# Kernel tuning notes

Hardware: AMD Instinct MI355X
Metric: run time of the kernel (lower is better)

The kernel has to match this reference:

```python
import jax, jax.numpy as jnp
import numpy as np

NEG_INF = -9e15
ALPHA = 0.2  # LeakyReLU negative slope

N = 8192
D_IN = 512
D_OUT = 256


def setup_inputs() -> dict:
    key = jax.random.key(0)
    k1, k2, k3, k4, k5 = jax.random.split(key, 5)
    features = jax.random.normal(k1, (N, D_IN), dtype=jnp.float32)
    adjacency_matrix = jax.random.randint(k2, (N, N), 0, 2, dtype=jnp.int32)
    # learned params (torch Linear stores [out, in]; we use [in, out] layout)
    s_phi = 1.0 / np.sqrt(D_IN)
    W_phi = jax.random.uniform(k3, (D_IN, D_OUT), jnp.float32, -s_phi, s_phi)
    s_v = 1.0 / np.sqrt(D_OUT)
    w_mu = jax.random.uniform(k4, (D_OUT,), jnp.float32, -s_v, s_v)
    w_xi = jax.random.uniform(k5, (D_OUT,), jnp.float32, -s_v, s_v)
    return {"features": features, "adjacency_matrix": adjacency_matrix,
            "W_phi": W_phi, "w_mu": w_mu, "w_xi": w_xi}


def reference(features, adjacency_matrix, W_phi, w_mu, w_xi):
    h = features @ W_phi                                   # [N, d_out]
    mu = h @ w_mu                                          # [N]
    xi = h @ w_xi                                          # [N]
    e = mu[:, None] + xi[None, :]                          # [N, N] additive scores
    e = jnp.where(e >= 0, e, ALPHA * e)                    # LeakyReLU
    e = jnp.where(adjacency_matrix > 0, e, NEG_INF)        # mask non-edges
    a = jax.nn.softmax(e, axis=1)                          # row softmax (dropout p=0)
    out = a @ h                                            # weighted aggregation
    return jax.nn.elu(out)
```

## Files before the change

### kernel.cpp

```cpp
#include <hip/hip_runtime.h>
#include <cstdint>
#include <cstddef>


#define LOG2E 1.44269504f

typedef __attribute__((ext_vector_type(8))) short short8;
typedef __attribute__((ext_vector_type(4))) float floatx4;

using uint_as1 = __attribute__((address_space(1))) unsigned int;
using uint_as3 = __attribute__((address_space(3))) unsigned int;

__device__ __forceinline__ void gld_lds16(const void* g, void* l) {
  __builtin_amdgcn_global_load_lds((const uint_as1*)g, (uint_as3*)l, 16, 0, 0);
}

__device__ __forceinline__ unsigned short f2b(float f) {
  unsigned u = __float_as_uint(f);
  u += 0x7fffu + ((u >> 16) & 1u);
  return (unsigned short)(u >> 16);
}

__device__ __forceinline__ unsigned cvtpk_bf16(float a, float b) {
  unsigned r;
  asm("v_cvt_pk_bf16_f32 %0, %1, %2" : "=v"(r) : "v"(a), "v"(b));
  return r;
}

__global__ void k_prep_wt(const float* __restrict__ w, unsigned short* __restrict__ wt) {
  int tid = blockIdx.x * 256 + threadIdx.x;
  int n = tid >> 9, k = tid & 511;
  wt[n * 512 + k] = f2b(w[k * 256 + n]);
}

__global__ __launch_bounds__(256, 2) void k_gemm1m(const float* __restrict__ f,
                                                   const unsigned short* __restrict__ wt,
                                                   const float* __restrict__ wmu,
                                                   const float* __restrict__ wxi,
                                                   unsigned short* __restrict__ ht,
                                                   float* __restrict__ mupart,
                                                   float* __restrict__ xipart) {
  __shared__ __align__(16) unsigned short As[64 * 64];
  __shared__ __align__(16) unsigned short Bs[128 * 64];
  __shared__ float musum[4][64];
  __shared__ float xisum[4][64];
  int t = threadIdx.x, w = t >> 6, l = t & 63;
  int bm_ = blockIdx.x >> 1, bn = blockIdx.x & 1;
  int m0 = bm_ * 64, n0 = bn * 128;
  int lr = l >> 3, lg = l & 7, g = lg ^ lr;
  int kg = l >> 4, ln = l & 15;
  floatx4 zero = {0.f, 0.f, 0.f, 0.f};
  floatx4 acc[4][2];
#pragma unroll
  for (int mf = 0; mf < 4; ++mf)
#pragma unroll
    for (int nf = 0; nf < 2; ++nf) acc[mf][nf] = zero;

  for (int it = 0; it < 8; ++it) {
    int k0 = it * 64;
#pragma unroll
    for (int q = 0; q < 2; ++q) {
      int row = w * 16 + q * 8 + lr;
      const float* fp = f + (size_t)(m0 + row) * 512 + k0 + g * 8;
      float4 v0 = *(const float4*)fp;
      float4 v1 = *(const float4*)(fp + 4);
      uint4 d = {cvtpk_bf16(v0.x, v0.y), cvtpk_bf16(v0.z, v0.w),
                 cvtpk_bf16(v1.x, v1.y), cvtpk_bf16(v1.z, v1.w)};
      *(uint4*)&As[row * 64 + lg * 8] = d;
    }
#pragma unroll
    for (int q = 0; q < 4; ++q) {
      int row = w * 32 + q * 8 + lr;
      const void* gp = wt + (size_t)(n0 + row) * 512 + k0 + g * 8;
      int lb = __builtin_amdgcn_readfirstlane((w * 32 + q * 8) * 64);
      gld_lds16(gp, &Bs[lb]);
    }
    __syncthreads();
#pragma unroll
    for (int ks = 0; ks < 2; ++ks) {
      int gg = ks * 4 + kg;
      int swz = (gg ^ (ln & 7)) * 8;
      short8 bfr[2];
#pragma unroll
      for (int nf = 0; nf < 2; ++nf)
        bfr[nf] = *(const short8*)&Bs[(w * 32 + nf * 16 + ln) * 64 + swz];
#pragma unroll
      for (int mf = 0; mf < 4; ++mf) {
        short8 afr = *(const short8*)&As[(mf * 16 + ln) * 64 + swz];
#pragma unroll
        for (int nf = 0; nf < 2; ++nf)
          acc[mf][nf] = __builtin_amdgcn_mfma_f32_16x16x32_bf16(afr, bfr[nf], acc[mf][nf], 0, 0, 0);
      }
    }
    __syncthreads();
  }
#pragma unroll
  for (int mf = 0; mf < 4; ++mf)
#pragma unroll
    for (int nf = 0; nf < 2; ++nf) {
      int ng = n0 + w * 32 + nf * 16 + ln;
      int mg = m0 + mf * 16 + kg * 4;
      ushort4 o = {f2b(acc[mf][nf][0]), f2b(acc[mf][nf][1]),
                   f2b(acc[mf][nf][2]), f2b(acc[mf][nf][3])};
      *(ushort4*)&ht[(size_t)ng * 8192 + mg] = o;
    }
  float wma = wmu[n0 + w * 32 + ln], wmb = wmu[n0 + w * 32 + 16 + ln];
  float wxa = wxi[n0 + w * 32 + ln], wxb = wxi[n0 + w * 32 + 16 + ln];
#pragma unroll
  for (int mf = 0; mf < 4; ++mf)
#pragma unroll
    for (int r = 0; r < 4; ++r) {
      float ms = acc[mf][0][r] * wma + acc[mf][1][r] * wmb;
      float xs = acc[mf][0][r] * wxa + acc[mf][1][r] * wxb;
      ms += __shfl_xor(ms, 1); ms += __shfl_xor(ms, 2);
      ms += __shfl_xor(ms, 4); ms += __shfl_xor(ms, 8);
      xs += __shfl_xor(xs, 1); xs += __shfl_xor(xs, 2);
      xs += __shfl_xor(xs, 4); xs += __shfl_xor(xs, 8);
      if (ln == 0) {
        musum[w][mf * 16 + kg * 4 + r] = ms;
        xisum[w][mf * 16 + kg * 4 + r] = xs;
      }
    }
  __syncthreads();
  if (t < 64) {
    float m_ = musum[0][t] + musum[1][t] + musum[2][t] + musum[3][t];
    mupart[(size_t)bn * 8192 + m0 + t] = m_;
  } else if (t < 128) {
    int r = t - 64;
    float x_ = xisum[0][r] + xisum[1][r] + xisum[2][r] + xisum[3][r];
    xipart[(size_t)bn * 8192 + m0 + r] = x_;
  }
}

__global__ __launch_bounds__(512, 1) void k_gatt16(const int* __restrict__ adjm,
                                                   const unsigned short* __restrict__ ht,
                                                   const float* __restrict__ mupart,
                                                   const float* __restrict__ xipart,
                                                   float* __restrict__ nump,
                                                   float* __restrict__ zpart) {
  __shared__ __align__(16) unsigned short Bs[4][256 * 32];
  __shared__ __align__(16) float EfE[1024];
  __shared__ __align__(16) float EfF[1024];

  int t = threadIdx.x, w = t >> 6, l = t & 63;
  int ln = l & 15, kg = l >> 4;
  int jb = blockIdx.x & 7, ig = blockIdx.x >> 3;
  int i0 = ig * 256;
  int jc0 = jb * 1024;

  {
    int t2 = t & 255;
    float4 xa = *(const float4*)&xipart[jc0 + t2 * 4];
    float4 xb = *(const float4*)&xipart[8192 + jc0 + t2 * 4];
    float x0 = (xa.x + xb.x) * LOG2E, x1 = (xa.y + xb.y) * LOG2E;
    float x2 = (xa.z + xb.z) * LOG2E, x3 = (xa.w + xb.w) * LOG2E;
    if (t < 256) {
      EfE[t2 * 4 + 0] = __builtin_amdgcn_exp2f(x0);
      EfE[t2 * 4 + 1] = __builtin_amdgcn_exp2f(x1);
      EfE[t2 * 4 + 2] = __builtin_amdgcn_exp2f(x2);
      EfE[t2 * 4 + 3] = __builtin_amdgcn_exp2f(x3);
    } else {
      EfF[t2 * 4 + 0] = __builtin_amdgcn_exp2f(0.2f * x0);
      EfF[t2 * 4 + 1] = __builtin_amdgcn_exp2f(0.2f * x1);
      EfF[t2 * 4 + 2] = __builtin_amdgcn_exp2f(0.2f * x2);
      EfF[t2 * 4 + 3] = __builtin_amdgcn_exp2f(0.2f * x3);
    }
  }

  float EM[2], FM[2];
#pragma unroll
  for (int mf = 0; mf < 2; ++mf) {
    int i = i0 + w * 32 + mf * 16 + ln;
    float mu = (mupart[i] + mupart[8192 + i]) * LOG2E;
    EM[mf] = __builtin_amdgcn_exp2f(mu);
    FM[mf] = __builtin_amdgcn_exp2f(0.2f * mu);
  }

  const int* ar0 = adjm + (size_t)(i0 + w * 32 + ln) * 8192 + jc0 + kg * 8;
  const int* ar1 = ar0 + (size_t)16 * 8192;

  floatx4 zero = {0.f, 0.f, 0.f, 0.f};
  floatx4 acc[2][16];
#pragma unroll
  for (int mf = 0; mf < 2; ++mf)
#pragma unroll
    for (int nf = 0; nf < 16; ++nf) acc[mf][nf] = zero;
  float zacc[2] = {0.f, 0.f};

#define STAGE_B(win_, b_)                                                   \
  {                                                                         \
    int j0_ = jc0 + (win_) * 32;                                            \
    _Pragma("unroll")                                                       \
    for (int q = 0; q < 2; ++q) {                                           \
      int rowbase = w * 32 + q * 16;                                        \
      int row = rowbase + (l >> 2);                                         \
      int g = (l & 3) ^ ((row >> 1) & 3);                                   \
      const void* gp = ht + (size_t)row * 8192 + j0_ + g * 8;               \
      int lb = __builtin_amdgcn_readfirstlane((b_) * (256 * 32) + rowbase * 32); \
      gld_lds16(gp, &((unsigned short*)Bs)[lb]);                            \
    }                                                                       \
  }

  STAGE_B(0, 0);
  STAGE_B(1, 1);
  __syncthreads();

  for (int win = 0; win < 32; ++win) {
    int bR = win & 3;
    if (win < 31) {
      asm volatile("s_waitcnt vmcnt(2)" ::: "memory");
    } else {
      asm volatile("s_waitcnt vmcnt(0)" ::: "memory");
    }
    __builtin_amdgcn_s_barrier();
    asm volatile("" ::: "memory");

    int joff = win * 32;
    int4 a0 = *(const int4*)(ar0 + joff);
    int4 a1 = *(const int4*)(ar0 + joff + 4);
    int4 a2 = *(const int4*)(ar1 + joff);
    int4 a3 = *(const int4*)(ar1 + joff + 4);

    int jl = win * 32 + kg * 8;
    float4 e0 = *(const float4*)&EfE[jl];
    float4 e1 = *(const float4*)&EfE[jl + 4];
    float4 f0 = *(const float4*)&EfF[jl];
    float4 f1 = *(const float4*)&EfF[jl + 4];

    short8 af[2];
#pragma unroll
    for (int mf = 0; mf < 2; ++mf) {
      int av[8];
      if (mf == 0) {
        av[0] = a0.x; av[1] = a0.y; av[2] = a0.z; av[3] = a0.w;
        av[4] = a1.x; av[5] = a1.y; av[6] = a1.z; av[7] = a1.w;
      } else {
        av[0] = a2.x; av[1] = a2.y; av[2] = a2.z; av[3] = a2.w;
        av[4] = a3.x; av[5] = a3.y; av[6] = a3.z; av[7] = a3.w;
      }
      float ex[8] = {e0.x, e0.y, e0.z, e0.w, e1.x, e1.y, e1.z, e1.w};
      float fx[8] = {f0.x, f0.y, f0.z, f0.w, f1.x, f1.y, f1.z, f1.w};
      float A = EM[mf], F = FM[mf];
      union { unsigned u[4]; short8 s; } cv;
      float zs = 0.f;
#pragma unroll
      for (int p = 0; p < 4; ++p) {
        float m0 = fmaxf(A * ex[2 * p], F * fx[2 * p]);
        float m1 = fmaxf(A * ex[2 * p + 1], F * fx[2 * p + 1]);
        m0 = (av[2 * p] != 0) ? m0 : 0.f;
        m1 = (av[2 * p + 1] != 0) ? m1 : 0.f;
        zs += m0;
        zs += m1;
        cv.u[p] = cvtpk_bf16(m0, m1);
      }
      zacc[mf] += zs;
      af[mf] = cv.s;
    }
#pragma unroll
    for (int qtr = 0; qtr < 4; ++qtr) {
      short8 bfv[4];
#pragma unroll
      for (int nf = 0; nf < 4; ++nf) {
        int n = qtr * 64 + nf * 16 + ln;
        bfv[nf] = *(const short8*)&Bs[bR][n * 32 + ((kg ^ ((n >> 1) & 3)) * 8)];
      }
#pragma unroll
      for (int mf = 0; mf < 2; ++mf)
#pragma unroll
        for (int nf = 0; nf < 4; ++nf)
          acc[mf][qtr * 4 + nf] = __builtin_amdgcn_mfma_f32_16x16x32_bf16(
              af[mf], bfv[nf], acc[mf][qtr * 4 + nf], 0, 0, 0);
    }
    if (win < 30) {
      STAGE_B(win + 2, (win + 2) & 3);
    }
  }
#undef STAGE_B

#pragma unroll
  for (int mf = 0; mf < 2; ++mf) {
    float z = zacc[mf];
    z += __shfl_xor(z, 16);
    z += __shfl_xor(z, 32);
    if (l < 16) zpart[(size_t)jb * 8192 + i0 + w * 32 + mf * 16 + ln] = z;
  }

  float* np = nump + (size_t)jb * (8192 * 256);
#pragma unroll
  for (int mf = 0; mf < 2; ++mf) {
    int rowb = i0 + w * 32 + mf * 16 + kg * 4;
#pragma unroll
    for (int r = 0; r < 4; ++r) {
      float* rp = np + (size_t)(rowb + r) * 256;
#pragma unroll
      for (int nf = 0; nf < 16; ++nf)
        rp[nf * 16 + ln] = acc[mf][nf][r];
    }
  }
}

__global__ void k_final(const float* __restrict__ nump, const float* __restrict__ zpart,
                        float* __restrict__ out) {
  int tid = blockIdx.x * 256 + threadIdx.x;
  int i = tid >> 6;
  float z = 0.f;
#pragma unroll
  for (int p = 0; p < 8; ++p) z += zpart[(size_t)p * 8192 + i];
  float zi = 1.0f / z;
  float4 v = {0.f, 0.f, 0.f, 0.f};
#pragma unroll
  for (int p = 0; p < 8; ++p) {
    float4 s = *(const float4*)&nump[(size_t)p * (8192 * 256) + tid * 4];
    v.x += s.x; v.y += s.y; v.z += s.z; v.w += s.w;
  }
  v.x *= zi; v.y *= zi; v.z *= zi; v.w *= zi;
  v.x = (v.x > 0.f) ? v.x : (__builtin_amdgcn_exp2f(v.x * LOG2E) - 1.f);
  v.y = (v.y > 0.f) ? v.y : (__builtin_amdgcn_exp2f(v.y * LOG2E) - 1.f);
  v.z = (v.z > 0.f) ? v.z : (__builtin_amdgcn_exp2f(v.z * LOG2E) - 1.f);
  v.w = (v.w > 0.f) ? v.w : (__builtin_amdgcn_exp2f(v.w * LOG2E) - 1.f);
  *(float4*)&out[tid * 4] = v;
}

extern "C" void kernel_launch(void* const* d_in, const int* in_sizes, int n_in,
                              void* d_out, int out_size, void* d_ws, size_t ws_size,
                              hipStream_t stream) {
  const float* features = (const float*)d_in[0];
  const int* adjm = (const int*)d_in[1];
  const float* W_phi = (const float*)d_in[2];
  const float* w_mu = (const float*)d_in[3];
  const float* w_xi = (const float*)d_in[4];
  float* out = (float*)d_out;

  char* ws = (char*)d_ws;
  unsigned short* ht  = (unsigned short*)(ws + 0);
  unsigned short* wt  = (unsigned short*)(ws + 4194304);
  float* mupart = (float*)(ws + 4456448);
  float* xipart = (float*)(ws + 4521984);
  float* zpart  = (float*)(ws + 4587520);
  float* nump   = (float*)(ws + 8388608);

  k_prep_wt<<<512, 256, 0, stream>>>(W_phi, wt);
  k_gemm1m<<<256, 256, 0, stream>>>(features, wt, w_mu, w_xi, ht, mupart, xipart);
  k_gatt16<<<256, 512, 0, stream>>>(adjm, ht, mupart, xipart, nump, zpart);
  k_final<<<2048, 256, 0, stream>>>(nump, zpart, out);
}
```

Baseline: 447.7 us.

## Fuse split-K reduction and ELU into attention kernel with in-block wave split

Restructures the attention kernel so each block owns 32 rows and its 8 waves split the 8192-wide neighbour dimension, reducing partial accumulators through shared memory and applying normalization and ELU in-kernel. This removes the partial-numerator buffer writes (8×8192×256 floats), the global zpart round trip and the separate final kernel launch. B fragments are now read directly from global memory without LDS staging, adjacency loads are software-prefetched one step ahead, and the whole exp table is rebuilt per block. Risks: uncached global B loads per MFMA, a serialized multi-step LDS tree reduction, and a single wave doing the final output writes.

```diff
diff --git a/kernel.cpp b/kernel.cpp
--- a/kernel.cpp
+++ b/kernel.cpp
@@ -132,52 +132,48 @@
   }
 }
 
-__global__ __launch_bounds__(512, 1) void k_gatt16(const int* __restrict__ adjm,
+__global__ __launch_bounds__(512, 1) void k_gatt17(const int* __restrict__ adjm,
                                                    const unsigned short* __restrict__ ht,
                                                    const float* __restrict__ mupart,
                                                    const float* __restrict__ xipart,
-                                                   float* __restrict__ nump,
-                                                   float* __restrict__ zpart) {
-  __shared__ __align__(16) unsigned short Bs[4][256 * 32];
-  __shared__ __align__(16) float EfE[1024];
-  __shared__ __align__(16) float EfF[1024];
+                                                   float* __restrict__ out) {
+  __shared__ __align__(16) char smem[131072];
+  __shared__ __align__(16) float zb[8][32];
+  __shared__ float zinv_s[32];
+
+  float* EfE = (float*)smem;
+  float* EfF = (float*)(smem + 32768);
 
   int t = threadIdx.x, w = t >> 6, l = t & 63;
   int ln = l & 15, kg = l >> 4;
-  int jb = blockIdx.x & 7, ig = blockIdx.x >> 3;
-  int i0 = ig * 256;
-  int jc0 = jb * 1024;
-
-  {
-    int t2 = t & 255;
-    float4 xa = *(const float4*)&xipart[jc0 + t2 * 4];
-    float4 xb = *(const float4*)&xipart[8192 + jc0 + t2 * 4];
+  int i0 = blockIdx.x * 32;
+  int jw0 = w * 1024;
+
+#pragma unroll
+  for (int q = 0; q < 4; ++q) {
+    int idx = q * 2048 + t * 4;
+    float4 xa = *(const float4*)&xipart[idx];
+    float4 xb = *(const float4*)&xipart[8192 + idx];
     float x0 = (xa.x + xb.x) * LOG2E, x1 = (xa.y + xb.y) * LOG2E;
     float x2 = (xa.z + xb.z) * LOG2E, x3 = (xa.w + xb.w) * LOG2E;
-    if (t < 256) {
-      EfE[t2 * 4 + 0] = __builtin_amdgcn_exp2f(x0);
-      EfE[t2 * 4 + 1] = __builtin_amdgcn_exp2f(x1);
-      EfE[t2 * 4 + 2] = __builtin_amdgcn_exp2f(x2);
-      EfE[t2 * 4 + 3] = __builtin_amdgcn_exp2f(x3);
-    } else {
-      EfF[t2 * 4 + 0] = __builtin_amdgcn_exp2f(0.2f * x0);
-      EfF[t2 * 4 + 1] = __builtin_amdgcn_exp2f(0.2f * x1);
-      EfF[t2 * 4 + 2] = __builtin_amdgcn_exp2f(0.2f * x2);
-      EfF[t2 * 4 + 3] = __builtin_amdgcn_exp2f(0.2f * x3);
-    }
-  }
-
+    EfE[idx + 0] = __builtin_amdgcn_exp2f(x0);
+    EfE[idx + 1] = __builtin_amdgcn_exp2f(x1);
+    EfE[idx + 2] = __builtin_amdgcn_exp2f(x2);
+    EfE[idx + 3] = __builtin_amdgcn_exp2f(x3);
+    EfF[idx + 0] = __builtin_amdgcn_exp2f(0.2f * x0);
+    EfF[idx + 1] = __builtin_amdgcn_exp2f(0.2f * x1);
+    EfF[idx + 2] = __builtin_amdgcn_exp2f(0.2f * x2);
+    EfF[idx + 3] = __builtin_amdgcn_exp2f(0.2f * x3);
+  }
   float EM[2], FM[2];
 #pragma unroll
   for (int mf = 0; mf < 2; ++mf) {
-    int i = i0 + w * 32 + mf * 16 + ln;
+    int i = i0 + mf * 16 + ln;
     float mu = (mupart[i] + mupart[8192 + i]) * LOG2E;
     EM[mf] = __builtin_amdgcn_exp2f(mu);
     FM[mf] = __builtin_amdgcn_exp2f(0.2f * mu);
   }
-
-  const int* ar0 = adjm + (size_t)(i0 + w * 32 + ln) * 8192 + jc0 + kg * 8;
-  const int* ar1 = ar0 + (size_t)16 * 8192;
+  __syncthreads();
 
   floatx4 zero = {0.f, 0.f, 0.f, 0.f};
   floatx4 acc[2][16];
@@ -187,56 +183,39 @@
     for (int nf = 0; nf < 16; ++nf) acc[mf][nf] = zero;
   float zacc[2] = {0.f, 0.f};
 
-#define STAGE_B(win_, b_)                                                   \
-  {                                                                         \
-    int j0_ = jc0 + (win_) * 32;                                            \
-    _Pragma("unroll")                                                       \
-    for (int q = 0; q < 2; ++q) {                                           \
-      int rowbase = w * 32 + q * 16;                                        \
-      int row = rowbase + (l >> 2);                                         \
-      int g = (l & 3) ^ ((row >> 1) & 3);                                   \
-      const void* gp = ht + (size_t)row * 8192 + j0_ + g * 8;               \
-      int lb = __builtin_amdgcn_readfirstlane((b_) * (256 * 32) + rowbase * 32); \
-      gld_lds16(gp, &((unsigned short*)Bs)[lb]);                            \
-    }                                                                       \
-  }
-
-  STAGE_B(0, 0);
-  STAGE_B(1, 1);
-  __syncthreads();
-
-  for (int win = 0; win < 32; ++win) {
-    int bR = win & 3;
-    if (win < 31) {
-      asm volatile("s_waitcnt vmcnt(2)" ::: "memory");
-    } else {
-      asm volatile("s_waitcnt vmcnt(0)" ::: "memory");
-    }
-    __builtin_amdgcn_s_barrier();
-    asm volatile("" ::: "memory");
-
-    int joff = win * 32;
-    int4 a0 = *(const int4*)(ar0 + joff);
-    int4 a1 = *(const int4*)(ar0 + joff + 4);
-    int4 a2 = *(const int4*)(ar1 + joff);
-    int4 a3 = *(const int4*)(ar1 + joff + 4);
-
-    int jl = win * 32 + kg * 8;
+  const int* ar0 = adjm + (size_t)(i0 + ln) * 8192 + jw0 + kg * 8;
+  const int* ar1 = ar0 + (size_t)16 * 8192;
+  const unsigned short* hb = ht + (size_t)ln * 8192 + jw0 + kg * 8;
+
+  int4 ac0 = *(const int4*)(ar0 + 0);
+  int4 ac1 = *(const int4*)(ar0 + 4);
+  int4 ac2 = *(const int4*)(ar1 + 0);
+  int4 ac3 = *(const int4*)(ar1 + 4);
+
+  for (int ks = 0; ks < 32; ++ks) {
+    int joff = ks * 32;
+    int jl = jw0 + joff + kg * 8;
     float4 e0 = *(const float4*)&EfE[jl];
     float4 e1 = *(const float4*)&EfE[jl + 4];
     float4 f0 = *(const float4*)&EfF[jl];
     float4 f1 = *(const float4*)&EfF[jl + 4];
-
+    int4 an0, an1, an2, an3;
+    if (ks < 31) {
+      an0 = *(const int4*)(ar0 + joff + 32);
+      an1 = *(const int4*)(ar0 + joff + 36);
+      an2 = *(const int4*)(ar1 + joff + 32);
+      an3 = *(const int4*)(ar1 + joff + 36);
+    }
     short8 af[2];
 #pragma unroll
     for (int mf = 0; mf < 2; ++mf) {
       int av[8];
       if (mf == 0) {
-        av[0] = a0.x; av[1] = a0.y; av[2] = a0.z; av[3] = a0.w;
-        av[4] = a1.x; av[5] = a1.y; av[6] = a1.z; av[7] = a1.w;
+        av[0] = ac0.x; av[1] = ac0.y; av[2] = ac0.z; av[3] = ac0.w;
+        av[4] = ac1.x; av[5] = ac1.y; av[6] = ac1.z; av[7] = ac1.w;
       } else {
-        av[0] = a2.x; av[1] = a2.y; av[2] = a2.z; av[3] = a2.w;
-        av[4] = a3.x; av[5] = a3.y; av[6] = a3.z; av[7] = a3.w;
+        av[0] = ac2.x; av[1] = ac2.y; av[2] = ac2.z; av[3] = ac2.w;
+        av[4] = ac3.x; av[5] = ac3.y; av[6] = ac3.z; av[7] = ac3.w;
       }
       float ex[8] = {e0.x, e0.y, e0.z, e0.w, e1.x, e1.y, e1.z, e1.w};
       float fx[8] = {f0.x, f0.y, f0.z, f0.w, f1.x, f1.y, f1.z, f1.w};
@@ -260,10 +239,8 @@
     for (int qtr = 0; qtr < 4; ++qtr) {
       short8 bfv[4];
 #pragma unroll
-      for (int nf = 0; nf < 4; ++nf) {
-        int n = qtr * 64 + nf * 16 + ln;
-        bfv[nf] = *(const short8*)&Bs[bR][n * 32 + ((kg ^ ((n >> 1) & 3)) * 8)];
-      }
+      for (int nf = 0; nf < 4; ++nf)
+        bfv[nf] = *(const short8*)&hb[(size_t)(qtr * 64 + nf * 16) * 8192 + joff];
 #pragma unroll
       for (int mf = 0; mf < 2; ++mf)
 #pragma unroll
@@ -271,54 +248,69 @@
           acc[mf][qtr * 4 + nf] = __builtin_amdgcn_mfma_f32_16x16x32_bf16(
               af[mf], bfv[nf], acc[mf][qtr * 4 + nf], 0, 0, 0);
     }
-    if (win < 30) {
-      STAGE_B(win + 2, (win + 2) & 3);
-    }
-  }
-#undef STAGE_B
+    ac0 = an0; ac1 = an1; ac2 = an2; ac3 = an3;
+  }
 
 #pragma unroll
   for (int mf = 0; mf < 2; ++mf) {
     float z = zacc[mf];
     z += __shfl_xor(z, 16);
     z += __shfl_xor(z, 32);
-    if (l < 16) zpart[(size_t)jb * 8192 + i0 + w * 32 + mf * 16 + ln] = z;
-  }
-
-  float* np = nump + (size_t)jb * (8192 * 256);
-#pragma unroll
-  for (int mf = 0; mf < 2; ++mf) {
-    int rowb = i0 + w * 32 + mf * 16 + kg * 4;
-#pragma unroll
-    for (int r = 0; r < 4; ++r) {
-      float* rp = np + (size_t)(rowb + r) * 256;
+    if (l < 16) zb[w][mf * 16 + l] = z;
+  }
+  __syncthreads();
+  if (t < 32) {
+    float z = 0.f;
+#pragma unroll
+    for (int p = 0; p < 8; ++p) z += zb[p][t];
+    zinv_s[t] = 1.0f / z;
+  }
+
+  float* red = (float*)smem;
+#define RED_W(slot_)                                                        \
+  {                                                                         \
+    float* dst = red + (slot_) * 8192;                                      \
+    _Pragma("unroll")                                                       \
+    for (int mf = 0; mf < 2; ++mf)                                          \
+      _Pragma("unroll")                                                     \
+      for (int nf = 0; nf < 16; ++nf)                                       \
+        *(floatx4*)&dst[(mf * 16 + nf) * 256 + l * 4] = acc[mf][nf];        \
+  }
+#define RED_R(slot_)                                                        \
+  {                                                                         \
+    const float* src = red + (slot_) * 8192;                                \
+    _Pragma("unroll")                                                       \
+    for (int mf = 0; mf < 2; ++mf)                                          \
+      _Pragma("unroll")                                                     \
+      for (int nf = 0; nf < 16; ++nf)                                       \
+        acc[mf][nf] += *(const floatx4*)&src[(mf * 16 + nf) * 256 + l * 4]; \
+  }
+  if (w >= 4) RED_W(w - 4);
+  __syncthreads();
+  if (w < 4) RED_R(w);
+  __syncthreads();
+  if (w == 2 || w == 3) RED_W(w - 2);
+  __syncthreads();
+  if (w < 2) RED_R(w);
+  __syncthreads();
+  if (w == 1) RED_W(0);
+  __syncthreads();
+  if (w == 0) {
+    RED_R(0);
+#pragma unroll
+    for (int mf = 0; mf < 2; ++mf)
 #pragma unroll
       for (int nf = 0; nf < 16; ++nf)
-        rp[nf * 16 + ln] = acc[mf][nf][r];
-    }
-  }
-}
-
-__global__ void k_final(const float* __restrict__ nump, const float* __restrict__ zpart,
-                        float* __restrict__ out) {
-  int tid = blockIdx.x * 256 + threadIdx.x;
-  int i = tid >> 6;
-  float z = 0.f;
-#pragma unroll
-  for (int p = 0; p < 8; ++p) z += zpart[(size_t)p * 8192 + i];
-  float zi = 1.0f / z;
-  float4 v = {0.f, 0.f, 0.f, 0.f};
-#pragma unroll
-  for (int p = 0; p < 8; ++p) {
-    float4 s = *(const float4*)&nump[(size_t)p * (8192 * 256) + tid * 4];
-    v.x += s.x; v.y += s.y; v.z += s.z; v.w += s.w;
-  }
-  v.x *= zi; v.y *= zi; v.z *= zi; v.w *= zi;
-  v.x = (v.x > 0.f) ? v.x : (__builtin_amdgcn_exp2f(v.x * LOG2E) - 1.f);
-  v.y = (v.y > 0.f) ? v.y : (__builtin_amdgcn_exp2f(v.y * LOG2E) - 1.f);
-  v.z = (v.z > 0.f) ? v.z : (__builtin_amdgcn_exp2f(v.z * LOG2E) - 1.f);
-  v.w = (v.w > 0.f) ? v.w : (__builtin_amdgcn_exp2f(v.w * LOG2E) - 1.f);
-  *(float4*)&out[tid * 4] = v;
+#pragma unroll
+        for (int r = 0; r < 4; ++r) {
+          int row = mf * 16 + kg * 4 + r;
+          float val = acc[mf][nf][r] * zinv_s[row];
+          val = (val > 0.f) ? val : (__builtin_amdgcn_exp2f(val * LOG2E) - 1.f);
+          out[(size_t)(i0 + row) * 256 + nf * 16 + ln] = val;
+        }
+  }
+#undef RED_W
+#undef RED_R
 }
 
 extern "C" void kernel_launch(void* const* d_in, const int* in_sizes, int n_in,
@@ -336,11 +328,8 @@
   unsigned short* wt  = (unsigned short*)(ws + 4194304);
   float* mupart = (float*)(ws + 4456448);
   float* xipart = (float*)(ws + 4521984);
-  float* zpart  = (float*)(ws + 4587520);
-  float* nump   = (float*)(ws + 8388608);
 
   k_prep_wt<<<512, 256, 0, stream>>>(W_phi, wt);
   k_gemm1m<<<256, 256, 0, stream>>>(features, wt, w_mu, w_xi, ht, mupart, xipart);
-  k_gatt16<<<256, 512, 0, stream>>>(adjm, ht, mupart, xipart, nump, zpart);
-  k_final<<<2048, 256, 0, stream>>>(nump, zpart, out);
-}
+  k_gatt17<<<256, 512, 0, stream>>>(adjm, ht, mupart, xipart, out);
+}
```

New measurement: 509.0 us. +13.7%, slower.

## Preload adjacency tile as ballot bitmasks in LDS before main loop

Applied to the files above, without the earlier changes.

Instead of each lane loading strided int4 adjacency values inside every window iteration, each wave now reads its 32 rows × 1024 columns coalesced up front and compresses them to 64-bit ballot bitmasks stored in shared memory. The main loop then extracts mask bits from LDS. The aim is coalesced adjacency loads and removing global-memory latency from the MFMA loop. The cost is a serialized prologue that loads the whole 1MB tile per block before compute starts, with no overlap, plus 32KB of extra LDS.

```diff
diff --git a/kernel.cpp b/kernel.cpp
--- a/kernel.cpp
+++ b/kernel.cpp
@@ -132,13 +132,14 @@
   }
 }
 
-__global__ __launch_bounds__(512, 1) void k_gatt16(const int* __restrict__ adjm,
+__global__ __launch_bounds__(512, 1) void k_gatt18(const int* __restrict__ adjm,
                                                    const unsigned short* __restrict__ ht,
                                                    const float* __restrict__ mupart,
                                                    const float* __restrict__ xipart,
                                                    float* __restrict__ nump,
                                                    float* __restrict__ zpart) {
   __shared__ __align__(16) unsigned short Bs[4][256 * 32];
+  __shared__ __align__(16) unsigned long long bitsA[4][4][256];
   __shared__ __align__(16) float EfE[1024];
   __shared__ __align__(16) float EfF[1024];
 
@@ -176,9 +177,6 @@
     FM[mf] = __builtin_amdgcn_exp2f(0.2f * mu);
   }
 
-  const int* ar0 = adjm + (size_t)(i0 + w * 32 + ln) * 8192 + jc0 + kg * 8;
-  const int* ar1 = ar0 + (size_t)16 * 8192;
-
   floatx4 zero = {0.f, 0.f, 0.f, 0.f};
   floatx4 acc[2][16];
 #pragma unroll
@@ -203,6 +201,35 @@
 
   STAGE_B(0, 0);
   STAGE_B(1, 1);
+
+  {
+    const int* rp_base = adjm + (size_t)(i0 + w * 32) * 8192 + jc0;
+    for (int r8 = 0; r8 < 32; ++r8) {
+      const int* rp = rp_base + (size_t)r8 * 8192;
+      int4 v0 = *(const int4*)(rp + 4 * l);
+      int4 v1 = *(const int4*)(rp + 256 + 4 * l);
+      int4 v2 = *(const int4*)(rp + 512 + 4 * l);
+      int4 v3 = *(const int4*)(rp + 768 + 4 * l);
+      int row = w * 32 + r8;
+#define BALLOT4(vv, ch)                                                     \
+      {                                                                     \
+        unsigned long long b0 = __ballot(vv.x != 0);                        \
+        unsigned long long b1 = __ballot(vv.y != 0);                        \
+        unsigned long long b2 = __ballot(vv.z != 0);                        \
+        unsigned long long b3 = __ballot(vv.w != 0);                        \
+        if (l < 4) {                                                        \
+          unsigned long long bs = (l == 0) ? b0 : (l == 1) ? b1             \
+                                  : (l == 2) ? b2 : b3;                     \
+          bitsA[ch][l][row] = bs;                                           \
+        }                                                                   \
+      }
+      BALLOT4(v0, 0)
+      BALLOT4(v1, 1)
+      BALLOT4(v2, 2)
+      BALLOT4(v3, 3)
+#undef BALLOT4
+    }
+  }
   __syncthreads();
 
   for (int win = 0; win < 32; ++win) {
@@ -215,43 +242,43 @@
     __builtin_amdgcn_s_barrier();
     asm volatile("" ::: "memory");
 
-    int joff = win * 32;
-    int4 a0 = *(const int4*)(ar0 + joff);
-    int4 a1 = *(const int4*)(ar0 + joff + 4);
-    int4 a2 = *(const int4*)(ar1 + joff);
-    int4 a3 = *(const int4*)(ar1 + joff + 4);
-
     int jl = win * 32 + kg * 8;
     float4 e0 = *(const float4*)&EfE[jl];
     float4 e1 = *(const float4*)&EfE[jl + 4];
     float4 f0 = *(const float4*)&EfF[jl];
     float4 f1 = *(const float4*)&EfF[jl + 4];
 
+    int j0 = win * 32 + kg * 8;
+    int chunk = j0 >> 8;
+    int p = (j0 & 255) >> 2;
+
     short8 af[2];
 #pragma unroll
     for (int mf = 0; mf < 2; ++mf) {
+      int row_local = w * 32 + mf * 16 + ln;
+      unsigned long long q0 = bitsA[chunk][0][row_local] >> p;
+      unsigned long long q1 = bitsA[chunk][1][row_local] >> p;
+      unsigned long long q2 = bitsA[chunk][2][row_local] >> p;
+      unsigned long long q3 = bitsA[chunk][3][row_local] >> p;
       int av[8];
-      if (mf == 0) {
-        av[0] = a0.x; av[1] = a0.y; av[2] = a0.z; av[3] = a0.w;
-        av[4] = a1.x; av[5] = a1.y; av[6] = a1.z; av[7] = a1.w;
-      } else {
-        av[0] = a2.x; av[1] = a2.y; av[2] = a2.z; av[3] = a2.w;
-        av[4] = a3.x; av[5] = a3.y; av[6] = a3.z; av[7] = a3.w;
-      }
+      av[0] = (int)(q0 & 1); av[1] = (int)(q1 & 1);
+      av[2] = (int)(q2 & 1); av[3] = (int)(q3 & 1);
+      av[4] = (int)((q0 >> 1) & 1); av[5] = (int)((q1 >> 1) & 1);
+      av[6] = (int)((q2 >> 1) & 1); av[7] = (int)((q3 >> 1) & 1);
       float ex[8] = {e0.x, e0.y, e0.z, e0.w, e1.x, e1.y, e1.z, e1.w};
       float fx[8] = {f0.x, f0.y, f0.z, f0.w, f1.x, f1.y, f1.z, f1.w};
       float A = EM[mf], F = FM[mf];
       union { unsigned u[4]; short8 s; } cv;
       float zs = 0.f;
 #pragma unroll
-      for (int p = 0; p < 4; ++p) {
-        float m0 = fmaxf(A * ex[2 * p], F * fx[2 * p]);
-        float m1 = fmaxf(A * ex[2 * p + 1], F * fx[2 * p + 1]);
-        m0 = (av[2 * p] != 0) ? m0 : 0.f;
-        m1 = (av[2 * p + 1] != 0) ? m1 : 0.f;
+      for (int pp = 0; pp < 4; ++pp) {
+        float m0 = fmaxf(A * ex[2 * pp], F * fx[2 * pp]);
+        float m1 = fmaxf(A * ex[2 * pp + 1], F * fx[2 * pp + 1]);
+        m0 = (av[2 * pp] != 0) ? m0 : 0.f;
+        m1 = (av[2 * pp + 1] != 0) ? m1 : 0.f;
         zs += m0;
         zs += m1;
-        cv.u[p] = cvtpk_bf16(m0, m1);
+        cv.u[pp] = cvtpk_bf16(m0, m1);
       }
       zacc[mf] += zs;
       af[mf] = cv.s;
@@ -341,6 +368,6 @@
 
   k_prep_wt<<<512, 256, 0, stream>>>(W_phi, wt);
   k_gemm1m<<<256, 256, 0, stream>>>(features, wt, w_mu, w_xi, ht, mupart, xipart);
-  k_gatt16<<<256, 512, 0, stream>>>(adjm, ht, mupart, xipart, nump, zpart);
+  k_gatt18<<<256, 512, 0, stream>>>(adjm, ht, mupart, xipart, nump, zpart);
   k_final<<<2048, 256, 0, stream>>>(nump, zpart, out);
 }
```

New measurement: 445.0 us. About the same (-0.6%).
